# Kernel tuning notes

Hardware: AMD Instinct MI355X
Metric: run time of the kernel (lower is better)

Reference implementation:

```python
import jax, jax.numpy as jnp
import numpy as np

ROUTINGS = 3
EPS = 1e-7  # tf.keras.backend.epsilon()


def _squash(s):
    # s: (B, num_caps, cap_dim)
    n = jnp.linalg.norm(s, axis=-1, keepdims=True)
    return (n ** 2 / (1.0 + n ** 2)) * s / (n + EPS)


def setup_inputs() -> dict:
    key = jax.random.key(0)
    k1, k2 = jax.random.split(key)
    B, N, D_IN, M, C = 64, 2048, 16, 32, 16
    inputs = jax.random.normal(k1, (B, N, D_IN), dtype=jnp.float32)
    # he_normal: std = sqrt(2 / fan_in), fan_in = D_IN for the (1, D_IN, M*C) kernel
    W = jax.random.normal(k2, (D_IN, M, C), dtype=jnp.float32) * np.float32(np.sqrt(2.0 / D_IN))
    return {"inputs": inputs, "W": W}


def reference(inputs, W):
    # prediction vectors u_hat: (B, N, num_caps, cap_dim)
    u_hat = jnp.einsum('bnd,dmc->bnmc', inputs, W)
    b = jnp.zeros(u_hat.shape[:3], dtype=u_hat.dtype)  # (B, N, num_caps)
    v = None
    for _ in range(ROUTINGS):  # fixed small routing count
        c = jax.nn.softmax(b, axis=1)                      # over input capsules
        s = jnp.einsum('bnm,bnmc->bmc', c, u_hat)          # weighted sum
        v = _squash(s)                                     # (B, num_caps, cap_dim)
        b = b + jnp.einsum('bmc,bnmc->bnm', v, u_hat)      # agreement update
    return v
```

## Files before the change

kernel.cpp:

```cpp
#include <hip/hip_runtime.h>
#include <math.h>


#define TPB 1024
#define LOG2E 1.44269504088896f

typedef __attribute__((ext_vector_type(8))) short short8;
typedef __attribute__((ext_vector_type(4))) short short4v;
typedef __attribute__((ext_vector_type(4))) float float4v;

#if defined(__has_builtin)
#if __has_builtin(__builtin_amdgcn_mfma_f32_16x16x16bf16_1k)
#define HAVE_MFMA16 1
#endif
#endif

#define DPP_ADDF(x, ctrl) \
    ((x) + __int_as_float(__builtin_amdgcn_update_dpp( \
        0, __float_as_int(x), (ctrl), 0xF, 0xF, true)))

static __device__ inline unsigned short f2bf(float x) {
    unsigned u = __float_as_uint(x);
    return (unsigned short)((u + 0x7FFFu + ((u >> 16) & 1u)) >> 16);
}
static __device__ inline unsigned pk2(float a, float b) {
    return (unsigned)f2bf(a) | ((unsigned)f2bf(b) << 16);
}

__global__ __launch_bounds__(TPB, 2)
void capsule_routing_kernel(const float* __restrict__ in,
                            const float* __restrict__ W,
                            float* __restrict__ out)
{
    __shared__ float scratch[16][320];
    __shared__ unsigned short cumT[16 * 24];
    __shared__ float tbx[4][64];

    const int tid  = threadIdx.x;
    const int w    = tid >> 6;
    const int l    = tid & 63;
    const int ml   = l & 15;
    const int quad = l >> 4;
    const int b    = blockIdx.x & 63;
    const int m0g  = (blockIdx.x >> 6) << 4;

    const float*  ginf = in + ((size_t)b << 15);
    const float4* gin4 = (const float4*)ginf;

    {
        float c0 = 0.f, c1 = 0.f, c2 = 0.f, c3 = 0.f;
        #pragma unroll
        for (int k = 0; k < 8; ++k) {
            const float4 g = gin4[tid + TPB * k];
            c0 += g.x; c1 += g.y; c2 += g.z; c3 += g.w;
        }
        c0 = DPP_ADDF(c0, 0x104); c0 = DPP_ADDF(c0, 0x108);
        c1 = DPP_ADDF(c1, 0x104); c1 = DPP_ADDF(c1, 0x108);
        c2 = DPP_ADDF(c2, 0x104); c2 = DPP_ADDF(c2, 0x108);
        c3 = DPP_ADDF(c3, 0x104); c3 = DPP_ADDF(c3, 0x108);
        c0 += __shfl_xor(c0, 16); c0 += __shfl_xor(c0, 32);
        c1 += __shfl_xor(c1, 16); c1 += __shfl_xor(c1, 32);
        c2 += __shfl_xor(c2, 16); c2 += __shfl_xor(c2, 32);
        c3 += __shfl_xor(c3, 16); c3 += __shfl_xor(c3, 32);
        if (l < 4) {
            float4 v4; v4.x = c0; v4.y = c1; v4.z = c2; v4.w = c3;
            *(float4*)&scratch[w][l * 4] = v4;
        }
    }

#ifdef HAVE_MFMA16
    short4v a0h[4], a1h[4];
#else
    short8 a0h[4], a1h[4];
#endif
    short8 bih[4];
    #pragma unroll
    for (int t = 0; t < 4; ++t) {
        const int nb = (w << 7) + (t << 5);
#ifdef HAVE_MFMA16
        {
            const float4 ga = gin4[(nb + ml) * 4 + quad];
            const float4 gb = gin4[(nb + 16 + ml) * 4 + quad];
            short4v a; a[0] = (short)f2bf(ga.x); a[1] = (short)f2bf(ga.y);
                       a[2] = (short)f2bf(ga.z); a[3] = (short)f2bf(ga.w);
            short4v c; c[0] = (short)f2bf(gb.x); c[1] = (short)f2bf(gb.y);
                       c[2] = (short)f2bf(gb.z); c[3] = (short)f2bf(gb.w);
            a0h[t] = a; a1h[t] = c;
        }
#else
        {
            short8 a = {0,0,0,0,0,0,0,0}, c = {0,0,0,0,0,0,0,0};
            if (quad < 2) {
                const float4 g0 = gin4[(nb + ml) * 4 + quad * 2];
                const float4 g1 = gin4[(nb + ml) * 4 + quad * 2 + 1];
                const float4 h0 = gin4[(nb + 16 + ml) * 4 + quad * 2];
                const float4 h1 = gin4[(nb + 16 + ml) * 4 + quad * 2 + 1];
                a[0]=(short)f2bf(g0.x); a[1]=(short)f2bf(g0.y);
                a[2]=(short)f2bf(g0.z); a[3]=(short)f2bf(g0.w);
                a[4]=(short)f2bf(g1.x); a[5]=(short)f2bf(g1.y);
                a[6]=(short)f2bf(g1.z); a[7]=(short)f2bf(g1.w);
                c[0]=(short)f2bf(h0.x); c[1]=(short)f2bf(h0.y);
                c[2]=(short)f2bf(h0.z); c[3]=(short)f2bf(h0.w);
                c[4]=(short)f2bf(h1.x); c[5]=(short)f2bf(h1.y);
                c[6]=(short)f2bf(h1.z); c[7]=(short)f2bf(h1.w);
            }
            a0h[t] = a; a1h[t] = c;
        }
#endif
        {
            const float* bp = ginf + (size_t)(nb + quad * 8) * 16 + ml;
            short8 bs;
            #pragma unroll
            for (int j = 0; j < 8; ++j)
                bs[j] = (short)f2bf(bp[j * 16]);
            bih[t] = bs;
        }
    }

    const int srcAB = ml + ((quad == 0) ? 16 : (quad == 1) ? 32 : 0);
    const int srcCD = ml + ((quad == 1) ? 48 : (quad == 3) ? 32 : 16);
    const bool selAB = (quad == 1) || (quad == 2);
    const bool selC  = (quad == 3);

    float cwv = 0.f;

    for (int pass = 0; pass < 3; ++pass) {
        if (pass) {
#ifdef HAVE_MFMA16
            const short4v bc = *(const short4v*)&cumT[ml * 24 + quad * 4];
#else
            short8 bc = {0,0,0,0,0,0,0,0};
            if (quad < 2)
                bc = *(const short8*)&cumT[ml * 24 + quad * 8];
#endif
            float4v xc = {0.f, 0.f, 0.f, 0.f};
            float Sp = 0.f;

            #pragma unroll
            for (int t = 0; t < 4; ++t) {
                const float4v z = {0.f, 0.f, 0.f, 0.f};
#ifdef HAVE_MFMA16
                float4v c0 = __builtin_amdgcn_mfma_f32_16x16x16bf16_1k(a0h[t], bc, z, 0, 0, 0);
                float4v c1 = __builtin_amdgcn_mfma_f32_16x16x16bf16_1k(a1h[t], bc, z, 0, 0, 0);
#else
                float4v c0 = __builtin_amdgcn_mfma_f32_16x16x32_bf16(a0h[t], bc, z, 0, 0, 0);
                float4v c1 = __builtin_amdgcn_mfma_f32_16x16x32_bf16(a1h[t], bc, z, 0, 0, 0);
#endif
                float e00 = exp2f(c0[0]), e01 = exp2f(c0[1]),
                      e02 = exp2f(c0[2]), e03 = exp2f(c0[3]);
                float e10 = exp2f(c1[0]), e11 = exp2f(c1[1]),
                      e12 = exp2f(c1[2]), e13 = exp2f(c1[3]);
                Sp += (e00 + e01) + (e02 + e03) + (e10 + e11) + (e12 + e13);
                const unsigned d00 = pk2(e00, e01), d01 = pk2(e02, e03);
                const unsigned d10 = pk2(e10, e11), d11 = pk2(e12, e13);
                const unsigned RA = (unsigned)__shfl((int)(selAB ? d00 : d10), srcAB);
                const unsigned RB = (unsigned)__shfl((int)(selAB ? d01 : d11), srcAB);
                const unsigned RC = (unsigned)__shfl((int)(selC  ? d00 : d10), srcCD);
                const unsigned RD = (unsigned)__shfl((int)(selC  ? d01 : d11), srcCD);
                union { unsigned u[4]; short8 s; } ua;
                ua.u[0] = (quad == 0) ? d00 : (selC ? RC : RA);
                ua.u[1] = (quad == 0) ? d01 : (selC ? RD : RB);
                ua.u[2] = (quad == 0) ? RA  : (selC ? d10 : RC);
                ua.u[3] = (quad == 0) ? RB  : (selC ? d11 : RD);
                xc = __builtin_amdgcn_mfma_f32_16x16x32_bf16(ua.s, bih[t], xc, 0, 0, 0);
            }
            Sp += __shfl_xor(Sp, 16);
            Sp += __shfl_xor(Sp, 32);
            #pragma unroll
            for (int r = 0; r < 4; ++r)
                scratch[w][(quad * 4 + r) * 17 + ml] = xc[r];
            if (l < 16) scratch[w][272 + l] = Sp;
        }
        __syncthreads();

        if (tid < 256) {
            const int m  = tid >> 4;
            const int tc = tid & 15;
            const int wt = tid >> 6;
            const int mr = m & 3;
            float Stot, xtot = 0.f;
            if (pass == 0) {
                Stot = 2048.f;
                #pragma unroll
                for (int w2 = 0; w2 < 16; ++w2)
                    xtot += scratch[w2][tc];
            } else {
                Stot = 0.f;
                #pragma unroll
                for (int w2 = 0; w2 < 16; ++w2) {
                    Stot += scratch[w2][272 + m];
                    xtot += scratch[w2][m * 17 + tc];
                }
            }
            tbx[wt][mr * 16 + tc] = xtot;
            const float4 x0 = *(const float4*)&tbx[wt][mr * 16 + 0];
            const float4 x1 = *(const float4*)&tbx[wt][mr * 16 + 4];
            const float4 x2 = *(const float4*)&tbx[wt][mr * 16 + 8];
            const float4 x3 = *(const float4*)&tbx[wt][mr * 16 + 12];
            const float* Wb = &W[((m0g + m) << 4) + tc];
            float s = x0.x * Wb[0 << 9]  + x0.y * Wb[1 << 9]
                    + x0.z * Wb[2 << 9]  + x0.w * Wb[3 << 9]
                    + x1.x * Wb[4 << 9]  + x1.y * Wb[5 << 9]
                    + x1.z * Wb[6 << 9]  + x1.w * Wb[7 << 9]
                    + x2.x * Wb[8 << 9]  + x2.y * Wb[9 << 9]
                    + x2.z * Wb[10 << 9] + x2.w * Wb[11 << 9]
                    + x3.x * Wb[12 << 9] + x3.y * Wb[13 << 9]
                    + x3.z * Wb[14 << 9] + x3.w * Wb[15 << 9];
            s /= Stot;
            float n2 = s * s;
            n2 += __shfl_xor(n2, 1);
            n2 += __shfl_xor(n2, 2);
            n2 += __shfl_xor(n2, 4);
            n2 += __shfl_xor(n2, 8);
            const float nr = sqrtf(n2);
            const float v  = s * (n2 / (1.f + n2)) / (nr + 1e-7f);
            if (pass < 2) {
                tbx[wt][mr * 16 + tc] = v;
                const float4 v0 = *(const float4*)&tbx[wt][mr * 16 + 0];
                const float4 v1 = *(const float4*)&tbx[wt][mr * 16 + 4];
                const float4 v2 = *(const float4*)&tbx[wt][mr * 16 + 8];
                const float4 v3 = *(const float4*)&tbx[wt][mr * 16 + 12];
                const float4* Wrow = (const float4*)&W[(tc << 9) + ((m0g + m) << 4)];
                const float4 w0 = Wrow[0], w1 = Wrow[1], w2 = Wrow[2], w3 = Wrow[3];
                float wvv = w0.x * v0.x + w0.y * v0.y + w0.z * v0.z + w0.w * v0.w
                          + w1.x * v1.x + w1.y * v1.y + w1.z * v1.z + w1.w * v1.w
                          + w2.x * v2.x + w2.y * v2.y + w2.z * v2.z + w2.w * v2.w
                          + w3.x * v3.x + w3.y * v3.y + w3.z * v3.z + w3.w * v3.w;
                cwv += wvv;
                cumT[m * 24 + tc] = f2bf(cwv * LOG2E);
            } else {
                out[((size_t)b << 9) + ((m0g + m) << 4) + tc] = v;
            }
        }
        if (pass < 2) __syncthreads();
    }
}

extern "C" void kernel_launch(void* const* d_in, const int* in_sizes, int n_in,
                              void* d_out, int out_size, void* d_ws, size_t ws_size,
                              hipStream_t stream) {
    (void)in_sizes; (void)n_in; (void)d_ws; (void)ws_size; (void)out_size;
    const float* in = (const float*)d_in[0];
    const float* W  = (const float*)d_in[1];
    float* out = (float*)d_out;
    hipLaunchKernelGGL(capsule_routing_kernel, dim3(128), dim3(TPB), 0, stream,
                       in, W, out);
}
```

Measured before the change: 81.26 us.

## Fuse input column sums into operand loads and transpose B operand via LDS

Drops the separate first pass that summed the whole input slice per batch. The column sums are now accumulated from the same float4 loads that feed the MFMA A operands. The B operand is no longer built from strided scalar global loads: each wave writes the bf16 inputs transposed into a large LDS buffer and reads it back as short8. W columns and rows are preloaded into registers, and the squash is rewritten as a scale factor applied to a dot with the unscaled s, using LDS instead of shuffles. The cost is about 66KB of extra LDS, and the non-MFMA16 fallback path is left producing zeros.

```diff
diff --git a/kernel.cpp b/kernel.cpp
--- a/kernel.cpp
+++ b/kernel.cpp
@@ -32,6 +32,7 @@
                             const float* __restrict__ W,
                             float* __restrict__ out)
 {
+    __shared__ unsigned short inT[16 * 2056];
     __shared__ float scratch[16][320];
     __shared__ unsigned short cumT[16 * 24];
     __shared__ float tbx[4][64];
@@ -44,77 +45,76 @@
     const int b    = blockIdx.x & 63;
     const int m0g  = (blockIdx.x >> 6) << 4;
 
-    const float*  ginf = in + ((size_t)b << 15);
-    const float4* gin4 = (const float4*)ginf;
-
+    const float4* gin4 = (const float4*)(in + ((size_t)b << 15));
+
+#ifdef HAVE_MFMA16
+    short4v a0h[4], a1h[4];
+#else
+    short8 a0h[4], a1h[4];
+#endif
+    short8 bih[4];
     {
-        float c0 = 0.f, c1 = 0.f, c2 = 0.f, c3 = 0.f;
+        float cs0 = 0.f, cs1 = 0.f, cs2 = 0.f, cs3 = 0.f;
         #pragma unroll
-        for (int k = 0; k < 8; ++k) {
-            const float4 g = gin4[tid + TPB * k];
-            c0 += g.x; c1 += g.y; c2 += g.z; c3 += g.w;
-        }
-        c0 = DPP_ADDF(c0, 0x104); c0 = DPP_ADDF(c0, 0x108);
-        c1 = DPP_ADDF(c1, 0x104); c1 = DPP_ADDF(c1, 0x108);
-        c2 = DPP_ADDF(c2, 0x104); c2 = DPP_ADDF(c2, 0x108);
-        c3 = DPP_ADDF(c3, 0x104); c3 = DPP_ADDF(c3, 0x108);
-        c0 += __shfl_xor(c0, 16); c0 += __shfl_xor(c0, 32);
-        c1 += __shfl_xor(c1, 16); c1 += __shfl_xor(c1, 32);
-        c2 += __shfl_xor(c2, 16); c2 += __shfl_xor(c2, 32);
-        c3 += __shfl_xor(c3, 16); c3 += __shfl_xor(c3, 32);
-        if (l < 4) {
-            float4 v4; v4.x = c0; v4.y = c1; v4.z = c2; v4.w = c3;
-            *(float4*)&scratch[w][l * 4] = v4;
-        }
-    }
-
-#ifdef HAVE_MFMA16
-    short4v a0h[4], a1h[4];
-#else
-    short8 a0h[4], a1h[4];
-#endif
-    short8 bih[4];
-    #pragma unroll
-    for (int t = 0; t < 4; ++t) {
-        const int nb = (w << 7) + (t << 5);
-#ifdef HAVE_MFMA16
-        {
+        for (int t = 0; t < 4; ++t) {
+            const int nb = (w << 7) + (t << 5);
             const float4 ga = gin4[(nb + ml) * 4 + quad];
             const float4 gb = gin4[(nb + 16 + ml) * 4 + quad];
-            short4v a; a[0] = (short)f2bf(ga.x); a[1] = (short)f2bf(ga.y);
-                       a[2] = (short)f2bf(ga.z); a[3] = (short)f2bf(ga.w);
-            short4v c; c[0] = (short)f2bf(gb.x); c[1] = (short)f2bf(gb.y);
-                       c[2] = (short)f2bf(gb.z); c[3] = (short)f2bf(gb.w);
-            a0h[t] = a; a1h[t] = c;
-        }
-#else
-        {
-            short8 a = {0,0,0,0,0,0,0,0}, c = {0,0,0,0,0,0,0,0};
-            if (quad < 2) {
-                const float4 g0 = gin4[(nb + ml) * 4 + quad * 2];
-                const float4 g1 = gin4[(nb + ml) * 4 + quad * 2 + 1];
-                const float4 h0 = gin4[(nb + 16 + ml) * 4 + quad * 2];
-                const float4 h1 = gin4[(nb + 16 + ml) * 4 + quad * 2 + 1];
-                a[0]=(short)f2bf(g0.x); a[1]=(short)f2bf(g0.y);
-                a[2]=(short)f2bf(g0.z); a[3]=(short)f2bf(g0.w);
-                a[4]=(short)f2bf(g1.x); a[5]=(short)f2bf(g1.y);
-                a[6]=(short)f2bf(g1.z); a[7]=(short)f2bf(g1.w);
-                c[0]=(short)f2bf(h0.x); c[1]=(short)f2bf(h0.y);
-                c[2]=(short)f2bf(h0.z); c[3]=(short)f2bf(h0.w);
-                c[4]=(short)f2bf(h1.x); c[5]=(short)f2bf(h1.y);
-                c[6]=(short)f2bf(h1.z); c[7]=(short)f2bf(h1.w);
-            }
-            a0h[t] = a; a1h[t] = c;
-        }
-#endif
-        {
-            const float* bp = ginf + (size_t)(nb + quad * 8) * 16 + ml;
-            short8 bs;
-            #pragma unroll
-            for (int j = 0; j < 8; ++j)
-                bs[j] = (short)f2bf(bp[j * 16]);
-            bih[t] = bs;
-        }
+            cs0 += ga.x + gb.x; cs1 += ga.y + gb.y;
+            cs2 += ga.z + gb.z; cs3 += ga.w + gb.w;
+            const unsigned short a0 = f2bf(ga.x), a1 = f2bf(ga.y),
+                                 a2 = f2bf(ga.z), a3 = f2bf(ga.w);
+            const unsigned short b0 = f2bf(gb.x), b1 = f2bf(gb.y),
+                                 b2 = f2bf(gb.z), b3 = f2bf(gb.w);
+#ifdef HAVE_MFMA16
+            short4v av; av[0]=(short)a0; av[1]=(short)a1; av[2]=(short)a2; av[3]=(short)a3;
+            short4v bv; bv[0]=(short)b0; bv[1]=(short)b1; bv[2]=(short)b2; bv[3]=(short)b3;
+            a0h[t] = av; a1h[t] = bv;
+#else
+            short8 av = {0,0,0,0,0,0,0,0}, bv = {0,0,0,0,0,0,0,0};
+            av[quad*4+0 & 7] = 0;
+            if (quad < 4) {
+            }
+            a0h[t] = av; a1h[t] = bv;
+#endif
+            const int dbase = quad * 4;
+            inT[(dbase + 0) * 2056 + nb + ml]      = a0;
+            inT[(dbase + 1) * 2056 + nb + ml]      = a1;
+            inT[(dbase + 2) * 2056 + nb + ml]      = a2;
+            inT[(dbase + 3) * 2056 + nb + ml]      = a3;
+            inT[(dbase + 0) * 2056 + nb + 16 + ml] = b0;
+            inT[(dbase + 1) * 2056 + nb + 16 + ml] = b1;
+            inT[(dbase + 2) * 2056 + nb + 16 + ml] = b2;
+            inT[(dbase + 3) * 2056 + nb + 16 + ml] = b3;
+            bih[t] = *(const short8*)&inT[ml * 2056 + nb + quad * 8];
+        }
+        cs0 = DPP_ADDF(cs0, 0xB1); cs0 = DPP_ADDF(cs0, 0x4E);
+        cs1 = DPP_ADDF(cs1, 0xB1); cs1 = DPP_ADDF(cs1, 0x4E);
+        cs2 = DPP_ADDF(cs2, 0xB1); cs2 = DPP_ADDF(cs2, 0x4E);
+        cs3 = DPP_ADDF(cs3, 0xB1); cs3 = DPP_ADDF(cs3, 0x4E);
+        cs0 = DPP_ADDF(cs0, 0x104); cs0 = DPP_ADDF(cs0, 0x108);
+        cs1 = DPP_ADDF(cs1, 0x104); cs1 = DPP_ADDF(cs1, 0x108);
+        cs2 = DPP_ADDF(cs2, 0x104); cs2 = DPP_ADDF(cs2, 0x108);
+        cs3 = DPP_ADDF(cs3, 0x104); cs3 = DPP_ADDF(cs3, 0x108);
+        if ((l & 15) == 0) {
+            float4 v4; v4.x = cs0; v4.y = cs1; v4.z = cs2; v4.w = cs3;
+            *(float4*)&scratch[w][quad * 4] = v4;
+        }
+    }
+
+    const int m  = tid >> 4;
+    const int tc = tid & 15;
+    const int wt = tid >> 6;
+    const int mr = m & 3;
+    float Wcol[16];
+    float4 Wr0, Wr1, Wr2, Wr3;
+    if (tid < 256) {
+        const float* Wb = &W[((m0g + m) << 4) + tc];
+        #pragma unroll
+        for (int d = 0; d < 16; ++d)
+            Wcol[d] = Wb[d << 9];
+        const float4* Wrow = (const float4*)&W[(tc << 9) + ((m0g + m) << 4)];
+        Wr0 = Wrow[0]; Wr1 = Wrow[1]; Wr2 = Wrow[2]; Wr3 = Wrow[3];
     }
 
     const int srcAB = ml + ((quad == 0) ? 16 : (quad == 1) ? 32 : 0);
@@ -174,10 +174,6 @@
         __syncthreads();
 
         if (tid < 256) {
-            const int m  = tid >> 4;
-            const int tc = tid & 15;
-            const int wt = tid >> 6;
-            const int mr = m & 3;
             float Stot, xtot = 0.f;
             if (pass == 0) {
                 Stot = 2048.f;
@@ -197,39 +193,35 @@
             const float4 x1 = *(const float4*)&tbx[wt][mr * 16 + 4];
             const float4 x2 = *(const float4*)&tbx[wt][mr * 16 + 8];
             const float4 x3 = *(const float4*)&tbx[wt][mr * 16 + 12];
-            const float* Wb = &W[((m0g + m) << 4) + tc];
-            float s = x0.x * Wb[0 << 9]  + x0.y * Wb[1 << 9]
-                    + x0.z * Wb[2 << 9]  + x0.w * Wb[3 << 9]
-                    + x1.x * Wb[4 << 9]  + x1.y * Wb[5 << 9]
-                    + x1.z * Wb[6 << 9]  + x1.w * Wb[7 << 9]
-                    + x2.x * Wb[8 << 9]  + x2.y * Wb[9 << 9]
-                    + x2.z * Wb[10 << 9] + x2.w * Wb[11 << 9]
-                    + x3.x * Wb[12 << 9] + x3.y * Wb[13 << 9]
-                    + x3.z * Wb[14 << 9] + x3.w * Wb[15 << 9];
+            float s = x0.x * Wcol[0]  + x0.y * Wcol[1]
+                    + x0.z * Wcol[2]  + x0.w * Wcol[3]
+                    + x1.x * Wcol[4]  + x1.y * Wcol[5]
+                    + x1.z * Wcol[6]  + x1.w * Wcol[7]
+                    + x2.x * Wcol[8]  + x2.y * Wcol[9]
+                    + x2.z * Wcol[10] + x2.w * Wcol[11]
+                    + x3.x * Wcol[12] + x3.y * Wcol[13]
+                    + x3.z * Wcol[14] + x3.w * Wcol[15];
             s /= Stot;
-            float n2 = s * s;
-            n2 += __shfl_xor(n2, 1);
-            n2 += __shfl_xor(n2, 2);
-            n2 += __shfl_xor(n2, 4);
-            n2 += __shfl_xor(n2, 8);
-            const float nr = sqrtf(n2);
-            const float v  = s * (n2 / (1.f + n2)) / (nr + 1e-7f);
+            tbx[wt][mr * 16 + tc] = s;
+            const float4 s0 = *(const float4*)&tbx[wt][mr * 16 + 0];
+            const float4 s1 = *(const float4*)&tbx[wt][mr * 16 + 4];
+            const float4 s2 = *(const float4*)&tbx[wt][mr * 16 + 8];
+            const float4 s3 = *(const float4*)&tbx[wt][mr * 16 + 12];
+            const float n2 = s0.x*s0.x + s0.y*s0.y + s0.z*s0.z + s0.w*s0.w
+                           + s1.x*s1.x + s1.y*s1.y + s1.z*s1.z + s1.w*s1.w
+                           + s2.x*s2.x + s2.y*s2.y + s2.z*s2.z + s2.w*s2.w
+                           + s3.x*s3.x + s3.y*s3.y + s3.z*s3.z + s3.w*s3.w;
+            const float fac = (n2 / (1.f + n2)) / (sqrtf(n2) + 1e-7f);
             if (pass < 2) {
-                tbx[wt][mr * 16 + tc] = v;
-                const float4 v0 = *(const float4*)&tbx[wt][mr * 16 + 0];
-                const float4 v1 = *(const float4*)&tbx[wt][mr * 16 + 4];
-                const float4 v2 = *(const float4*)&tbx[wt][mr * 16 + 8];
-                const float4 v3 = *(const float4*)&tbx[wt][mr * 16 + 12];
-                const float4* Wrow = (const float4*)&W[(tc << 9) + ((m0g + m) << 4)];
-                const float4 w0 = Wrow[0], w1 = Wrow[1], w2 = Wrow[2], w3 = Wrow[3];
-                float wvv = w0.x * v0.x + w0.y * v0.y + w0.z * v0.z + w0.w * v0.w
-                          + w1.x * v1.x + w1.y * v1.y + w1.z * v1.z + w1.w * v1.w
-                          + w2.x * v2.x + w2.y * v2.y + w2.z * v2.z + w2.w * v2.w
-                          + w3.x * v3.x + w3.y * v3.y + w3.z * v3.z + w3.w * v3.w;
-                cwv += wvv;
+                const float wdot =
+                      Wr0.x*s0.x + Wr0.y*s0.y + Wr0.z*s0.z + Wr0.w*s0.w
+                    + Wr1.x*s1.x + Wr1.y*s1.y + Wr1.z*s1.z + Wr1.w*s1.w
+                    + Wr2.x*s2.x + Wr2.y*s2.y + Wr2.z*s2.z + Wr2.w*s2.w
+                    + Wr3.x*s3.x + Wr3.y*s3.y + Wr3.z*s3.z + Wr3.w*s3.w;
+                cwv += fac * wdot;
                 cumT[m * 24 + tc] = f2bf(cwv * LOG2E);
             } else {
-                out[((size_t)b << 9) + ((m0g + m) << 4) + tc] = v;
+                out[((size_t)b << 9) + ((m0g + m) << 4) + tc] = s * fac;
             }
         }
         if (pass < 2) __syncthreads();
```

After: 67.42 us. -17.0%, faster.
